# Kernel tuning notes

Hardware: AMD Instinct MI355X
Metric: run time of the kernel (lower is better)

## Reference

```python
import jax, jax.numpy as jnp
import numpy as np

NUM_HEADS = 32
HEAD_DIM = 128
NUM_KV_HEADS = 8
SCALE = 0.08838834764831845  # 1/sqrt(128)
NUM_BLOCKS = 8192
BLOCK_SIZE = 16
BATCH = 64
MAX_BLOCKS = 128  # max context = 2048 tokens


def setup_inputs() -> dict:
    key = jax.random.key(0)
    k1, k2, k3, k4, k5 = jax.random.split(key, 5)
    q = jax.random.normal(k1, (BATCH, NUM_HEADS, HEAD_DIM), dtype=jnp.float32)
    k_cache = jax.random.normal(k2, (NUM_BLOCKS, BLOCK_SIZE, NUM_KV_HEADS, HEAD_DIM), dtype=jnp.float32)
    v_cache = jax.random.normal(k3, (NUM_BLOCKS, BLOCK_SIZE, NUM_KV_HEADS, HEAD_DIM), dtype=jnp.float32)
    block_tables = jax.random.randint(k4, (BATCH, MAX_BLOCKS), 0, NUM_BLOCKS, dtype=jnp.int32)
    # context lengths in [1, MAX_BLOCKS*BLOCK_SIZE] so no sequence is empty
    context_lens = jax.random.randint(k5, (BATCH,), 1, MAX_BLOCKS * BLOCK_SIZE + 1, dtype=jnp.int32)
    return {"q": q, "k_cache": k_cache, "v_cache": v_cache,
            "block_tables": block_tables, "context_lens": context_lens}


def reference(q, k_cache, v_cache, block_tables, context_lens):
    """Decode-phase paged attention with GQA.

    q:            [B, H, D]  one query token per sequence
    k_cache/v_cache: [num_blocks, block_size, KVH, D]
    block_tables: [B, M] int block ids (invalid entries masked by context_lens)
    context_lens: [B] valid KV length per sequence
    """
    B, H, D = q.shape
    _, bs, KVH, _ = k_cache.shape
    M = block_tables.shape[1]
    G = H // KVH  # query heads per kv head

    bt = jnp.maximum(block_tables, 0)  # invalid ids clamped; masked below
    # gather paged KV: [B, M, bs, KVH, D] -> [B, L, KVH, D], L = M*bs
    k = k_cache[bt].reshape(B, M * bs, KVH, D)
    v = v_cache[bt].reshape(B, M * bs, KVH, D)

    qr = q.reshape(B, KVH, G, D)
    logits = jnp.einsum('bvgd,blvd->bvgl', qr, k) * SCALE  # [B, KVH, G, L]

    valid = jnp.arange(M * bs)[None, :] < context_lens[:, None]  # [B, L]
    logits = jnp.where(valid[:, None, None, :], logits, -jnp.inf)

    attn = jax.nn.softmax(logits, axis=-1)
    out = jnp.einsum('bvgl,blvd->bvgd', attn, v)  # [B, KVH, G, D]
    return out.reshape(B, H, D)
```

## Files before the change

kernel.cpp:

```cpp
#include <hip/hip_runtime.h>

#define NBATCH 64
#define NHEADS 32
#define HDIM   128
#define NKVH   8
#define GQ     4
#define BLKSZ  16
#define MAXBLK 128
#define SCALE  0.08838834764831845f

__global__ __launch_bounds__(256, 2) void pa_decode(
    const float* __restrict__ q,
    const float* __restrict__ kc,
    const float* __restrict__ vc,
    const int*   __restrict__ block_tables,
    const int*   __restrict__ context_lens,
    float*       __restrict__ out)
{
    const int kvh  = blockIdx.x;
    const int b    = blockIdx.y;
    const int tid  = threadIdx.x;
    const int wave = tid >> 6;
    const int lane = tid & 63;
    const int half = lane >> 5;
    const int l32  = lane & 31;

    __shared__ int   s_bt[MAXBLK];
    __shared__ float s_m[4][GQ];
    __shared__ float s_l[4][GQ];
    __shared__ float s_acc[4][GQ][HDIM];

    const int L = context_lens[b];
    if (tid < MAXBLK) s_bt[tid] = block_tables[b * MAXBLK + tid];
    __syncthreads();

    float4 qv[GQ];
#pragma unroll
    for (int g = 0; g < GQ; ++g) {
        const float4 t = *(const float4*)(q + ((b * NHEADS + kvh * GQ + g) << 7) + 4 * l32);
        qv[g] = make_float4(t.x * SCALE, t.y * SCALE, t.z * SCALE, t.w * SCALE);
    }

    float  m[GQ], l[GQ];
    float4 acc[GQ];
#pragma unroll
    for (int g = 0; g < GQ; ++g) {
        m[g] = -__builtin_inff();
        l[g] = 0.f;
        acc[g] = make_float4(0.f, 0.f, 0.f, 0.f);
    }

    auto addr = [&](int t) -> int {
        const int blk = s_bt[t >> 4];
        return ((blk * BLKSZ + (t & 15)) * NKVH + kvh) * HDIM + 4 * l32;
    };

    const int tfirst = wave * 2 + half;
    float4 kcur, vcur;
    kcur = make_float4(0.f, 0.f, 0.f, 0.f);
    vcur = kcur;
    if (wave * 2 < L) {
        const int tt = (tfirst < L) ? tfirst : 0;
        const int o = addr(tt);
        kcur = *(const float4*)(kc + o);
        vcur = *(const float4*)(vc + o);
    }

    for (int base = 0; base + wave * 2 < L; base += 8) {
        const int  t     = base + wave * 2 + half;
        const bool valid = t < L;

        const int tn  = t + 8;
        const int ttn = (tn < L) ? tn : 0;
        const int on  = addr(ttn);
        const float4 knxt = *(const float4*)(kc + on);
        const float4 vnxt = *(const float4*)(vc + on);

        float s[GQ];
#pragma unroll
        for (int g = 0; g < GQ; ++g)
            s[g] = qv[g].x * kcur.x + qv[g].y * kcur.y + qv[g].z * kcur.z + qv[g].w * kcur.w;

#pragma unroll
        for (int d2 = 1; d2 < 32; d2 <<= 1) {
#pragma unroll
            for (int g = 0; g < GQ; ++g)
                s[g] += __shfl_xor(s[g], d2);
        }
        if (!valid) {
#pragma unroll
            for (int g = 0; g < GQ; ++g) s[g] = -__builtin_inff();
        }

#pragma unroll
        for (int g = 0; g < GQ; ++g) {
            const float so    = __shfl_xor(s[g], 32);
            const float mnew  = fmaxf(m[g], fmaxf(s[g], so));
            const float p     = __expf(s[g] - mnew);
            const float alpha = __expf(m[g] - mnew);
            m[g] = mnew;
            l[g] = l[g] * alpha + p;
            acc[g].x = acc[g].x * alpha + p * vcur.x;
            acc[g].y = acc[g].y * alpha + p * vcur.y;
            acc[g].z = acc[g].z * alpha + p * vcur.z;
            acc[g].w = acc[g].w * alpha + p * vcur.w;
        }
        kcur = knxt;
        vcur = vnxt;
    }

#pragma unroll
    for (int g = 0; g < GQ; ++g) {
        l[g]     += __shfl_xor(l[g], 32);
        acc[g].x += __shfl_xor(acc[g].x, 32);
        acc[g].y += __shfl_xor(acc[g].y, 32);
        acc[g].z += __shfl_xor(acc[g].z, 32);
        acc[g].w += __shfl_xor(acc[g].w, 32);
    }

    if (lane == 0) {
#pragma unroll
        for (int g = 0; g < GQ; ++g) { s_m[wave][g] = m[g]; s_l[wave][g] = l[g]; }
    }
    if (half == 0) {
#pragma unroll
        for (int g = 0; g < GQ; ++g)
            *(float4*)&s_acc[wave][g][4 * l32] = acc[g];
    }
    __syncthreads();

    for (int o = tid; o < GQ * HDIM; o += 256) {
        const int g = o >> 7;
        const int d = o & 127;
        const float mg = fmaxf(fmaxf(s_m[0][g], s_m[1][g]), fmaxf(s_m[2][g], s_m[3][g]));
        float num = 0.f, den = 0.f;
#pragma unroll
        for (int w = 0; w < 4; ++w) {
            const float sc = __expf(s_m[w][g] - mg);
            num += sc * s_acc[w][g][d];
            den += sc * s_l[w][g];
        }
        out[((b * NHEADS + kvh * GQ + g) << 7) + d] = num / den;
    }
}

extern "C" void kernel_launch(void* const* d_in, const int* in_sizes, int n_in,
                              void* d_out, int out_size, void* d_ws, size_t ws_size,
                              hipStream_t stream) {
    const float* q   = (const float*)d_in[0];
    const float* kc  = (const float*)d_in[1];
    const float* vc  = (const float*)d_in[2];
    const int*   bt  = (const int*)d_in[3];
    const int*   ctx = (const int*)d_in[4];
    float* out = (float*)d_out;

    dim3 grid(NKVH, NBATCH);
    pa_decode<<<grid, 256, 0, stream>>>(q, kc, vc, bt, ctx, out);
}
```

Measured before the change: 996.7 us.

## Split KV sequence into chunks across blocks with a separate reduction kernel

```diff
diff --git a/kernel.cpp b/kernel.cpp
--- a/kernel.cpp
+++ b/kernel.cpp
@@ -9,29 +9,39 @@
 #define MAXBLK 128
 #define SCALE  0.08838834764831845f
 
-__global__ __launch_bounds__(256, 2) void pa_decode(
+#define CHUNK  128
+#define NPARTS 16
+#define PART_STRIDE (GQ*HDIM + 2*GQ)
+
+__global__ __launch_bounds__(256, 4) void pa_partial(
     const float* __restrict__ q,
     const float* __restrict__ kc,
     const float* __restrict__ vc,
     const int*   __restrict__ block_tables,
     const int*   __restrict__ context_lens,
-    float*       __restrict__ out)
+    float*       __restrict__ part)
 {
-    const int kvh  = blockIdx.x;
-    const int b    = blockIdx.y;
+    const int kvh = blockIdx.x;
+    const int b   = blockIdx.y;
+    const int p   = blockIdx.z;
+    const int L   = context_lens[b];
+    const int start = p * CHUNK;
+    if (start >= L) return;
+    const int end = min(L, start + CHUNK);
+
     const int tid  = threadIdx.x;
     const int wave = tid >> 6;
     const int lane = tid & 63;
     const int half = lane >> 5;
     const int l32  = lane & 31;
 
-    __shared__ int   s_bt[MAXBLK];
+    __shared__ int   s_bt[CHUNK / BLKSZ];
     __shared__ float s_m[4][GQ];
     __shared__ float s_l[4][GQ];
     __shared__ float s_acc[4][GQ][HDIM];
 
-    const int L = context_lens[b];
-    if (tid < MAXBLK) s_bt[tid] = block_tables[b * MAXBLK + tid];
+    const int nblk = (end - start + BLKSZ - 1) / BLKSZ;
+    if (tid < nblk) s_bt[tid] = block_tables[b * MAXBLK + (start >> 4) + tid];
     __syncthreads();
 
     float4 qv[GQ];
@@ -51,62 +61,76 @@
     }
 
     auto addr = [&](int t) -> int {
-        const int blk = s_bt[t >> 4];
+        const int blk = s_bt[(t - start) >> 4];
         return ((blk * BLKSZ + (t & 15)) * NKVH + kvh) * HDIM + 4 * l32;
     };
-
-    const int tfirst = wave * 2 + half;
-    float4 kcur, vcur;
-    kcur = make_float4(0.f, 0.f, 0.f, 0.f);
-    vcur = kcur;
-    if (wave * 2 < L) {
-        const int tt = (tfirst < L) ? tfirst : 0;
-        const int o = addr(tt);
-        kcur = *(const float4*)(kc + o);
-        vcur = *(const float4*)(vc + o);
-    }
-
-    for (int base = 0; base + wave * 2 < L; base += 8) {
-        const int  t     = base + wave * 2 + half;
-        const bool valid = t < L;
-
-        const int tn  = t + 8;
-        const int ttn = (tn < L) ? tn : 0;
-        const int on  = addr(ttn);
-        const float4 knxt = *(const float4*)(kc + on);
-        const float4 vnxt = *(const float4*)(vc + on);
-
-        float s[GQ];
-#pragma unroll
-        for (int g = 0; g < GQ; ++g)
-            s[g] = qv[g].x * kcur.x + qv[g].y * kcur.y + qv[g].z * kcur.z + qv[g].w * kcur.w;
-
+    auto clampt = [&](int t) -> int { return t < end ? t : start; };
+
+    const int wbase = start + wave * 4;
+    float4 k0, k1, v0, v1;
+    if (wbase < end) {
+        const int a0 = addr(clampt(wbase + half * 2));
+        const int a1 = addr(clampt(wbase + half * 2 + 1));
+        k0 = *(const float4*)(kc + a0);
+        k1 = *(const float4*)(kc + a1);
+        v0 = *(const float4*)(vc + a0);
+        v1 = *(const float4*)(vc + a1);
+    }
+
+    for (int tb = wbase; tb < end; tb += 16) {
+        const int t0 = tb + half * 2;
+        const int t1 = t0 + 1;
+
+        float4 nk0, nk1, nv0, nv1;
+        const int nb = tb + 16;
+        if (nb < end) {
+            const int a0 = addr(clampt(nb + half * 2));
+            const int a1 = addr(clampt(nb + half * 2 + 1));
+            nk0 = *(const float4*)(kc + a0);
+            nk1 = *(const float4*)(kc + a1);
+            nv0 = *(const float4*)(vc + a0);
+            nv1 = *(const float4*)(vc + a1);
+        }
+
+        float s0[GQ], s1[GQ];
+#pragma unroll
+        for (int g = 0; g < GQ; ++g) {
+            s0[g] = qv[g].x * k0.x + qv[g].y * k0.y + qv[g].z * k0.z + qv[g].w * k0.w;
+            s1[g] = qv[g].x * k1.x + qv[g].y * k1.y + qv[g].z * k1.z + qv[g].w * k1.w;
+        }
 #pragma unroll
         for (int d2 = 1; d2 < 32; d2 <<= 1) {
 #pragma unroll
-            for (int g = 0; g < GQ; ++g)
-                s[g] += __shfl_xor(s[g], d2);
-        }
-        if (!valid) {
-#pragma unroll
-            for (int g = 0; g < GQ; ++g) s[g] = -__builtin_inff();
+            for (int g = 0; g < GQ; ++g) {
+                s0[g] += __shfl_xor(s0[g], d2);
+                s1[g] += __shfl_xor(s1[g], d2);
+            }
+        }
+        if (t0 >= end) {
+#pragma unroll
+            for (int g = 0; g < GQ; ++g) s0[g] = -__builtin_inff();
+        }
+        if (t1 >= end) {
+#pragma unroll
+            for (int g = 0; g < GQ; ++g) s1[g] = -__builtin_inff();
         }
 
 #pragma unroll
         for (int g = 0; g < GQ; ++g) {
-            const float so    = __shfl_xor(s[g], 32);
-            const float mnew  = fmaxf(m[g], fmaxf(s[g], so));
-            const float p     = __expf(s[g] - mnew);
-            const float alpha = __expf(m[g] - mnew);
+            const float o0 = __shfl_xor(s0[g], 32);
+            const float o1 = __shfl_xor(s1[g], 32);
+            const float mnew = fmaxf(m[g], fmaxf(fmaxf(s0[g], s1[g]), fmaxf(o0, o1)));
+            const float al = __expf(m[g] - mnew);
+            const float p0 = __expf(s0[g] - mnew);
+            const float p1 = __expf(s1[g] - mnew);
             m[g] = mnew;
-            l[g] = l[g] * alpha + p;
-            acc[g].x = acc[g].x * alpha + p * vcur.x;
-            acc[g].y = acc[g].y * alpha + p * vcur.y;
-            acc[g].z = acc[g].z * alpha + p * vcur.z;
-            acc[g].w = acc[g].w * alpha + p * vcur.w;
-        }
-        kcur = knxt;
-        vcur = vnxt;
+            l[g] = l[g] * al + p0 + p1;
+            acc[g].x = acc[g].x * al + p0 * v0.x + p1 * v1.x;
+            acc[g].y = acc[g].y * al + p0 * v0.y + p1 * v1.y;
+            acc[g].z = acc[g].z * al + p0 * v0.z + p1 * v1.z;
+            acc[g].w = acc[g].w * al + p0 * v0.w + p1 * v1.w;
+        }
+        k0 = nk0; k1 = nk1; v0 = nv0; v1 = nv1;
     }
 
 #pragma unroll
@@ -129,6 +153,7 @@
     }
     __syncthreads();
 
+    float* pp = part + (size_t)((b * NKVH + kvh) * NPARTS + p) * PART_STRIDE;
     for (int o = tid; o < GQ * HDIM; o += 256) {
         const int g = o >> 7;
         const int d = o & 127;
@@ -139,6 +164,48 @@
             const float sc = __expf(s_m[w][g] - mg);
             num += sc * s_acc[w][g][d];
             den += sc * s_l[w][g];
+        }
+        pp[g * HDIM + d] = num;
+        if (d == 0) {
+            pp[GQ * HDIM + g]      = mg;
+            pp[GQ * HDIM + GQ + g] = den;
+        }
+    }
+}
+
+__global__ __launch_bounds__(256) void pa_reduce(
+    const float* __restrict__ part,
+    const int*   __restrict__ context_lens,
+    float*       __restrict__ out)
+{
+    const int kvh = blockIdx.x;
+    const int b   = blockIdx.y;
+    const int L   = context_lens[b];
+    const int np  = (L + CHUNK - 1) / CHUNK;
+    const float* pb = part + (size_t)(b * NKVH + kvh) * NPARTS * PART_STRIDE;
+    const int tid = threadIdx.x;
+
+    __shared__ float sm[NPARTS][GQ];
+    __shared__ float sl[NPARTS][GQ];
+    if (tid < NPARTS * GQ) {
+        const int pi = tid >> 2, g = tid & 3;
+        if (pi < np) {
+            sm[pi][g] = pb[pi * PART_STRIDE + GQ * HDIM + g];
+            sl[pi][g] = pb[pi * PART_STRIDE + GQ * HDIM + GQ + g];
+        }
+    }
+    __syncthreads();
+
+    for (int o = tid; o < GQ * HDIM; o += 256) {
+        const int g = o >> 7;
+        const int d = o & 127;
+        float mg = -__builtin_inff();
+        for (int pi = 0; pi < np; ++pi) mg = fmaxf(mg, sm[pi][g]);
+        float num = 0.f, den = 0.f;
+        for (int pi = 0; pi < np; ++pi) {
+            const float sc = __expf(sm[pi][g] - mg);
+            num += sc * pb[pi * PART_STRIDE + g * HDIM + d];
+            den += sc * sl[pi][g];
         }
         out[((b * NHEADS + kvh * GQ + g) << 7) + d] = num / den;
     }
@@ -152,8 +219,12 @@
     const float* vc  = (const float*)d_in[2];
     const int*   bt  = (const int*)d_in[3];
     const int*   ctx = (const int*)d_in[4];
-    float* out = (float*)d_out;
-
-    dim3 grid(NKVH, NBATCH);
-    pa_decode<<<grid, 256, 0, stream>>>(q, kc, vc, bt, ctx, out);
+    float* out  = (float*)d_out;
+    float* part = (float*)d_ws;
+
+    dim3 grid1(NKVH, NBATCH, NPARTS);
+    pa_partial<<<grid1, 256, 0, stream>>>(q, kc, vc, bt, ctx, part);
+
+    dim3 grid2(NKVH, NBATCH);
+    pa_reduce<<<grid2, 256, 0, stream>>>(part, ctx, out);
 }
```

New measurement: 891.4 us. -10.6%, faster.
